# Performance work log

Hardware: AMD Instinct MI355X
Metric: run time of the kernel (lower is better)

## Reference

```python
import jax, jax.numpy as jnp
import numpy as np

TEMPERATURE = 0.5


def setup_inputs() -> dict:
    key = jax.random.key(0)
    k1, k2 = jax.random.split(key)
    emb_i = jax.random.normal(k1, (4096, 512), dtype=jnp.float32)
    emb_j = jax.random.normal(k2, (4096, 512), dtype=jnp.float32)
    return {"emb_i": emb_i, "emb_j": emb_j}


def reference(emb_i, emb_j):
    # NT-Xent (SimCLR) loss, vectorized over the original per-sample python loop.
    N = emb_i.shape[0]
    z_i = emb_i / jnp.linalg.norm(emb_i, axis=1, keepdims=True)
    z_j = emb_j / jnp.linalg.norm(emb_j, axis=1, keepdims=True)
    z = jnp.concatenate([z_i, z_j], axis=0)  # [2N, d]
    # cosine similarity of unit vectors == dot product
    sim = z @ z.T                             # [2N, 2N]
    exp_sim = jnp.exp(sim / TEMPERATURE)
    # denominator excludes self-similarity (the scatter-zero in the original)
    denom = exp_sim.sum(axis=1) - jnp.diagonal(exp_sim)
    idx = jnp.arange(2 * N)
    pos_idx = jnp.concatenate([jnp.arange(N) + N, jnp.arange(N)])
    num = exp_sim[idx, pos_idx]               # positive-pair similarities
    loss = -jnp.log(num / denom)
    return loss.mean()
```

## Files before the change

### kernel.cpp

```cpp
#include <hip/hip_runtime.h>
#include <hip/hip_bf16.h>

typedef __attribute__((ext_vector_type(4))) int i32x4;

#define AS1 __attribute__((address_space(1)))
#define AS3 __attribute__((address_space(3)))

#define DDIM 512
#define BK 64

__global__ __launch_bounds__(256) void norm_pd_kernel(
    const float* __restrict__ ei, const float* __restrict__ ej,
    unsigned char* __restrict__ zq, float* __restrict__ pd,
    float* __restrict__ rowsum, float* __restrict__ out, int N) {
  const int k = blockIdx.x * 4 + (threadIdx.x >> 6);
  const int l = threadIdx.x & 63;

  const float4 a0 = *reinterpret_cast<const float4*>(ei + (size_t)k * DDIM + l * 8);
  const float4 a1 = *reinterpret_cast<const float4*>(ei + (size_t)k * DDIM + l * 8 + 4);
  const float4 b0 = *reinterpret_cast<const float4*>(ej + (size_t)k * DDIM + l * 8);
  const float4 b1 = *reinterpret_cast<const float4*>(ej + (size_t)k * DDIM + l * 8 + 4);

  float sii = a0.x*a0.x + a0.y*a0.y + a0.z*a0.z + a0.w*a0.w
            + a1.x*a1.x + a1.y*a1.y + a1.z*a1.z + a1.w*a1.w;
  float sjj = b0.x*b0.x + b0.y*b0.y + b0.z*b0.z + b0.w*b0.w
            + b1.x*b1.x + b1.y*b1.y + b1.z*b1.z + b1.w*b1.w;
  float sij = a0.x*b0.x + a0.y*b0.y + a0.z*b0.z + a0.w*b0.w
            + a1.x*b1.x + a1.y*b1.y + a1.z*b1.z + a1.w*b1.w;
#pragma unroll
  for (int off = 32; off; off >>= 1) {
    sii += __shfl_xor(sii, off);
    sjj += __shfl_xor(sjj, off);
    sij += __shfl_xor(sij, off);
  }
  const float rsi = rsqrtf(sii), rsj = rsqrtf(sjj);

  unsigned char qa[8], qb[8];
  const float av[8] = {a0.x, a0.y, a0.z, a0.w, a1.x, a1.y, a1.z, a1.w};
  const float bv[8] = {b0.x, b0.y, b0.z, b0.w, b1.x, b1.y, b1.z, b1.w};
#pragma unroll
  for (int i = 0; i < 8; ++i) {
    qa[i] = (unsigned char)((int)rintf(127.0f * av[i] * rsi) & 0xff);
    qb[i] = (unsigned char)((int)rintf(127.0f * bv[i] * rsj) & 0xff);
  }
  *reinterpret_cast<uint2*>(zq + (size_t)k * DDIM + l * 8) =
      *reinterpret_cast<const uint2*>(qa);
  *reinterpret_cast<uint2*>(zq + (size_t)(N + k) * DDIM + l * 8) =
      *reinterpret_cast<const uint2*>(qb);
  if (l == 0) {
    pd[k] = sij * rsi * rsj;
    rowsum[k] = 0.0f;
    rowsum[N + k] = 0.0f;
    if (k == 0) out[0] = 0.0f;
  }
}


#define MFMAI8(A, B, C) __builtin_amdgcn_mfma_i32_16x16x64_i8((A), (B), (C), 0, 0, 0)

__global__ __launch_bounds__(256, 4) void simloss_main(
    const unsigned char* __restrict__ zq, float* __restrict__ rowsum, int nwg) {
  const int orig = blockIdx.x;
  const int q = nwg >> 3, r8 = nwg & 7;
  const int xcd = orig & 7, pos0 = orig >> 3;
  const int t0 = (xcd < r8 ? xcd * (q + 1) : r8 * (q + 1) + (xcd - r8) * q) + pos0;

  const float ff = sqrtf(8.0f * (float)t0 + 1.0f);
  int by = (int)((ff - 1.0f) * 0.5f);
  while ((by + 1) * (by + 2) / 2 <= t0) ++by;
  while (by * (by + 1) / 2 > t0) --by;
  const int bx = t0 - by * (by + 1) / 2;

  const int row0 = bx * 128;
  const int col0 = by * 128;

  __shared__ unsigned char lds[2][2][8192];

  const int tid = threadIdx.x;
  const int w = tid >> 6;
  const int l = tid & 63;
  const int wr = (w >> 1) * 64;
  const int wc = (w & 1) * 64;
  const int lrow = l & 15;
  const int g = l >> 4;

  i32x4 acc[4][4] = {};

  auto stage = [&](int buf, int k0) {
#pragma unroll
    for (int half = 0; half < 2; ++half) {
      const int baserow = half ? col0 : row0;
#pragma unroll
      for (int it = 0; it < 2; ++it) {
        const int pp = it * 256 + tid;
        const int row = pp >> 2;
        const int s = pp & 3;
        const int gs = (s - (row >> 1)) & 3;
        const unsigned char* src = zq + (size_t)(baserow + row) * DDIM + k0 + gs * 16;
        char* dst = (char*)&lds[buf][half][0] + (unsigned)((it * 256 + w * 64) * 16);
        __builtin_amdgcn_global_load_lds((const AS1 void*)src, (AS3 void*)dst, 16, 0, 0);
      }
    }
  };

  auto compute = [&](int buf) {
    const unsigned char* ab = &lds[buf][0][0];
    const unsigned char* bb = &lds[buf][1][0];
    i32x4 Af[4], Bf[4];
#pragma unroll
    for (int mf = 0; mf < 4; ++mf) {
      const int rr = wr + mf * 16 + lrow;
      Af[mf] = *reinterpret_cast<const i32x4*>(ab + rr * 64 + (((g + (rr >> 1)) & 3) << 4));
    }
#pragma unroll
    for (int nf = 0; nf < 4; ++nf) {
      const int cc = wc + nf * 16 + lrow;
      Bf[nf] = *reinterpret_cast<const i32x4*>(bb + cc * 64 + (((g + (cc >> 1)) & 3) << 4));
    }
#pragma unroll
    for (int mf = 0; mf < 4; ++mf)
#pragma unroll
      for (int nf = 0; nf < 4; ++nf)
        acc[mf][nf] = MFMAI8(Af[mf], Bf[nf], acc[mf][nf]);
  };

  stage(0, 0);

#pragma unroll
  for (int t = 0; t < 7; ++t) {
    const int buf = t & 1;
    stage(buf ^ 1, (t + 1) * BK);
    asm volatile("s_waitcnt vmcnt(4)" ::: "memory");
    __builtin_amdgcn_s_barrier();
    compute(buf);
    __builtin_amdgcn_s_barrier();
  }
  asm volatile("s_waitcnt vmcnt(0)" ::: "memory");
  __builtin_amdgcn_s_barrier();
  compute(1);

  const float SC = 2.0f * 1.44269504088896340736f / 16129.0f;
  const int lgrp = l >> 4;
  const int lcol = l & 15;

  float e[4][4][4];
#pragma unroll
  for (int mf = 0; mf < 4; ++mf)
#pragma unroll
    for (int nf = 0; nf < 4; ++nf)
#pragma unroll
      for (int rg = 0; rg < 4; ++rg)
        e[mf][nf][rg] = exp2f((float)acc[mf][nf][rg] * SC);

#pragma unroll
  for (int mf = 0; mf < 4; ++mf) {
    float rs[4];
#pragma unroll
    for (int rg = 0; rg < 4; ++rg) {
      float s = 0.0f;
#pragma unroll
      for (int nf = 0; nf < 4; ++nf) s += e[mf][nf][rg];
      rs[rg] = s;
    }
#pragma unroll
    for (int off = 1; off < 16; off <<= 1) {
#pragma unroll
      for (int rg = 0; rg < 4; ++rg) rs[rg] += __shfl_xor(rs[rg], off);
    }
    if (lcol == 0) {
      const int rowb = row0 + wr + mf * 16 + lgrp * 4;
#pragma unroll
      for (int rg = 0; rg < 4; ++rg) atomicAdd(&rowsum[rowb + rg], rs[rg]);
    }
  }

  if (bx != by) {
#pragma unroll
    for (int nf = 0; nf < 4; ++nf) {
      float cs = 0.0f;
#pragma unroll
      for (int mf = 0; mf < 4; ++mf)
#pragma unroll
        for (int rg = 0; rg < 4; ++rg) cs += e[mf][nf][rg];
      cs += __shfl_xor(cs, 16);
      cs += __shfl_xor(cs, 32);
      if (lgrp == 0) atomicAdd(&rowsum[col0 + wc + nf * 16 + lcol], cs);
    }
  }
}

__global__ __launch_bounds__(1024) void finalize_kernel(
    const float* __restrict__ rowsum, const float* __restrict__ pd,
    float* __restrict__ out, int M, int N) {
  const int i = blockIdx.x * 1024 + threadIdx.x;
  const float E2 = 7.38905609893065f;
  float acc = 0.0f;
  if (i < M) {
    const float denom = rowsum[i] - E2;
    const int kk = (i < N) ? i : (i - N);
    acc = logf(denom) - 2.0f * pd[kk];
  }
#pragma unroll
  for (int off = 32; off; off >>= 1) acc += __shfl_down(acc, off);
  __shared__ float red[16];
  const int t = threadIdx.x;
  if ((t & 63) == 0) red[t >> 6] = acc;
  __syncthreads();
  if (t < 64) {
    float s = (t < 16) ? red[t] : 0.0f;
#pragma unroll
    for (int off = 8; off; off >>= 1) s += __shfl_down(s, off);
    if (t == 0) atomicAdd(out, s / (float)M);
  }
}

extern "C" void kernel_launch(void* const* d_in, const int* in_sizes, int n_in,
                              void* d_out, int out_size, void* d_ws, size_t ws_size,
                              hipStream_t stream) {
  const float* ei = (const float*)d_in[0];
  const float* ej = (const float*)d_in[1];
  float* out = (float*)d_out;

  const int N = in_sizes[0] / DDIM;
  const int M = 2 * N;
  const int NT = M / 128;
  const int NTRI = NT * (NT + 1) / 2;

  char* ws = (char*)d_ws;
  unsigned char* zq = (unsigned char*)ws;
  float* pd = (float*)(ws + (size_t)M * DDIM);
  float* rowsum = (float*)(ws + (size_t)M * DDIM + (size_t)N * 4);

  norm_pd_kernel<<<N / 4, 256, 0, stream>>>(ei, ej, zq, pd, rowsum, out, N);
  simloss_main<<<NTRI, 256, 0, stream>>>(zq, rowsum, NTRI);
  finalize_kernel<<<(M + 1023) / 1024, 1024, 0, stream>>>(rowsum, pd, out, M, N);
}
```

Measured before the change: 44.43 us.

## Split 128x128 tile across 8 waves and fuse exp into row/column sums

Doubles the workgroup to 512 threads (8 waves in a 2x4 grid), so each wave computes a 64x32 sub-tile with half the accumulators. Each thread now issues one async global-to-LDS load per half-tile, and the wait count drops to match. The exponentials are computed inline into the row and column partial sums instead of being held in a 64-float array. This lowers register pressure and raises wave-level parallelism. In exchange, each wave does more LDS A-fragment loads relative to its MFMA work, and barriers must synchronise more waves.

Result: slower. 57.78 us (+30.1%).

```diff
diff --git a/kernel.cpp b/kernel.cpp
--- a/kernel.cpp
+++ b/kernel.cpp
@@ -58,7 +58,7 @@
 
 #define MFMAI8(A, B, C) __builtin_amdgcn_mfma_i32_16x16x64_i8((A), (B), (C), 0, 0, 0)
 
-__global__ __launch_bounds__(256, 4) void simloss_main(
+__global__ __launch_bounds__(512, 8) void simloss_main(
     const unsigned char* __restrict__ zq, float* __restrict__ rowsum, int nwg) {
   const int orig = blockIdx.x;
   const int q = nwg >> 3, r8 = nwg & 7;
@@ -79,48 +79,45 @@
   const int tid = threadIdx.x;
   const int w = tid >> 6;
   const int l = tid & 63;
-  const int wr = (w >> 1) * 64;
-  const int wc = (w & 1) * 64;
+  const int wr = (w >> 2) * 64;
+  const int wc = (w & 3) * 32;
   const int lrow = l & 15;
   const int g = l >> 4;
 
-  i32x4 acc[4][4] = {};
+  i32x4 acc[4][2] = {};
 
   auto stage = [&](int buf, int k0) {
 #pragma unroll
     for (int half = 0; half < 2; ++half) {
       const int baserow = half ? col0 : row0;
-#pragma unroll
-      for (int it = 0; it < 2; ++it) {
-        const int pp = it * 256 + tid;
-        const int row = pp >> 2;
-        const int s = pp & 3;
-        const int gs = (s - (row >> 1)) & 3;
-        const unsigned char* src = zq + (size_t)(baserow + row) * DDIM + k0 + gs * 16;
-        char* dst = (char*)&lds[buf][half][0] + (unsigned)((it * 256 + w * 64) * 16);
-        __builtin_amdgcn_global_load_lds((const AS1 void*)src, (AS3 void*)dst, 16, 0, 0);
-      }
+      const int c = w * 64 + l;
+      const int row = c >> 2;
+      const int s = c & 3;
+      const int gs = (s - (row >> 1)) & 3;
+      const unsigned char* src = zq + (size_t)(baserow + row) * DDIM + k0 + gs * 16;
+      char* dst = (char*)&lds[buf][half][0] + (unsigned)(w * 1024);
+      __builtin_amdgcn_global_load_lds((const AS1 void*)src, (AS3 void*)dst, 16, 0, 0);
     }
   };
 
   auto compute = [&](int buf) {
     const unsigned char* ab = &lds[buf][0][0];
     const unsigned char* bb = &lds[buf][1][0];
-    i32x4 Af[4], Bf[4];
+    i32x4 Af[4], Bf[2];
 #pragma unroll
     for (int mf = 0; mf < 4; ++mf) {
       const int rr = wr + mf * 16 + lrow;
       Af[mf] = *reinterpret_cast<const i32x4*>(ab + rr * 64 + (((g + (rr >> 1)) & 3) << 4));
     }
 #pragma unroll
-    for (int nf = 0; nf < 4; ++nf) {
+    for (int nf = 0; nf < 2; ++nf) {
       const int cc = wc + nf * 16 + lrow;
       Bf[nf] = *reinterpret_cast<const i32x4*>(bb + cc * 64 + (((g + (cc >> 1)) & 3) << 4));
     }
 #pragma unroll
     for (int mf = 0; mf < 4; ++mf)
 #pragma unroll
-      for (int nf = 0; nf < 4; ++nf)
+      for (int nf = 0; nf < 2; ++nf)
         acc[mf][nf] = MFMAI8(Af[mf], Bf[nf], acc[mf][nf]);
   };
 
@@ -130,7 +127,7 @@
   for (int t = 0; t < 7; ++t) {
     const int buf = t & 1;
     stage(buf ^ 1, (t + 1) * BK);
-    asm volatile("s_waitcnt vmcnt(4)" ::: "memory");
+    asm volatile("s_waitcnt vmcnt(2)" ::: "memory");
     __builtin_amdgcn_s_barrier();
     compute(buf);
     __builtin_amdgcn_s_barrier();
@@ -143,24 +140,17 @@
   const int lgrp = l >> 4;
   const int lcol = l & 15;
 
-  float e[4][4][4];
-#pragma unroll
-  for (int mf = 0; mf < 4; ++mf)
-#pragma unroll
-    for (int nf = 0; nf < 4; ++nf)
-#pragma unroll
-      for (int rg = 0; rg < 4; ++rg)
-        e[mf][nf][rg] = exp2f((float)acc[mf][nf][rg] * SC);
-
+  float cs0 = 0.0f, cs1 = 0.0f;
 #pragma unroll
   for (int mf = 0; mf < 4; ++mf) {
     float rs[4];
 #pragma unroll
     for (int rg = 0; rg < 4; ++rg) {
-      float s = 0.0f;
-#pragma unroll
-      for (int nf = 0; nf < 4; ++nf) s += e[mf][nf][rg];
-      rs[rg] = s;
+      const float e0 = exp2f((float)acc[mf][0][rg] * SC);
+      const float e1 = exp2f((float)acc[mf][1][rg] * SC);
+      rs[rg] = e0 + e1;
+      cs0 += e0;
+      cs1 += e1;
     }
 #pragma unroll
     for (int off = 1; off < 16; off <<= 1) {
@@ -175,16 +165,11 @@
   }
 
   if (bx != by) {
-#pragma unroll
-    for (int nf = 0; nf < 4; ++nf) {
-      float cs = 0.0f;
-#pragma unroll
-      for (int mf = 0; mf < 4; ++mf)
-#pragma unroll
-        for (int rg = 0; rg < 4; ++rg) cs += e[mf][nf][rg];
-      cs += __shfl_xor(cs, 16);
-      cs += __shfl_xor(cs, 32);
-      if (lgrp == 0) atomicAdd(&rowsum[col0 + wc + nf * 16 + lcol], cs);
+    cs0 += __shfl_xor(cs0, 16); cs0 += __shfl_xor(cs0, 32);
+    cs1 += __shfl_xor(cs1, 16); cs1 += __shfl_xor(cs1, 32);
+    if (lgrp == 0) {
+      atomicAdd(&rowsum[col0 + wc + lcol], cs0);
+      atomicAdd(&rowsum[col0 + wc + 16 + lcol], cs1);
     }
   }
 }
@@ -232,6 +217,6 @@
   float* rowsum = (float*)(ws + (size_t)M * DDIM + (size_t)N * 4);
 
   norm_pd_kernel<<<N / 4, 256, 0, stream>>>(ei, ej, zq, pd, rowsum, out, N);
-  simloss_main<<<NTRI, 256, 0, stream>>>(zq, rowsum, NTRI);
+  simloss_main<<<NTRI, 512, 0, stream>>>(zq, rowsum, NTRI);
   finalize_kernel<<<(M + 1023) / 1024, 1024, 0, stream>>>(rowsum, pd, out, M, N);
 }
```

## Enlarge similarity tiles to 256x256 with 512-thread blocks and fused epilogue

Applied to the files above, without the earlier changes.

Doubles the output tile of the triangular int8 similarity GEMM from 128x128 to 256x256, using 8 waves of 128x64 subtiles per block, and doubles the LDS staging buffers. Each wave's accumulator grows to 8x4 MFMA tiles. The epilogue now computes exp2 inline and accumulates row and column sums in one pass, dropping the full exp array to save registers. Bigger tiles cut global and LDS reload traffic and per-tile atomics, but give far fewer blocks (528 vs 2080) and lower occupancy, which risks leaving CUs underused.

New measurement: 59.11 us. 33.1% more time.

```diff
diff --git a/kernel.cpp b/kernel.cpp
--- a/kernel.cpp
+++ b/kernel.cpp
@@ -58,7 +58,7 @@
 
 #define MFMAI8(A, B, C) __builtin_amdgcn_mfma_i32_16x16x64_i8((A), (B), (C), 0, 0, 0)
 
-__global__ __launch_bounds__(256, 4) void simloss_main(
+__global__ __launch_bounds__(512, 2) void simloss_main(
     const unsigned char* __restrict__ zq, float* __restrict__ rowsum, int nwg) {
   const int orig = blockIdx.x;
   const int q = nwg >> 3, r8 = nwg & 7;
@@ -71,20 +71,20 @@
   while (by * (by + 1) / 2 > t0) --by;
   const int bx = t0 - by * (by + 1) / 2;
 
-  const int row0 = bx * 128;
-  const int col0 = by * 128;
-
-  __shared__ unsigned char lds[2][2][8192];
+  const int row0 = bx * 256;
+  const int col0 = by * 256;
+
+  __shared__ unsigned char lds[2][2][16384];
 
   const int tid = threadIdx.x;
   const int w = tid >> 6;
   const int l = tid & 63;
-  const int wr = (w >> 1) * 64;
-  const int wc = (w & 1) * 64;
+  const int wm = w >> 2;
+  const int wn = w & 3;
   const int lrow = l & 15;
   const int g = l >> 4;
 
-  i32x4 acc[4][4] = {};
+  i32x4 acc[8][4] = {};
 
   auto stage = [&](int buf, int k0) {
 #pragma unroll
@@ -92,12 +92,12 @@
       const int baserow = half ? col0 : row0;
 #pragma unroll
       for (int it = 0; it < 2; ++it) {
-        const int pp = it * 256 + tid;
+        const int pp = it * 512 + tid;
         const int row = pp >> 2;
         const int s = pp & 3;
         const int gs = (s - (row >> 1)) & 3;
         const unsigned char* src = zq + (size_t)(baserow + row) * DDIM + k0 + gs * 16;
-        char* dst = (char*)&lds[buf][half][0] + (unsigned)((it * 256 + w * 64) * 16);
+        char* dst = (char*)&lds[buf][half][0] + (unsigned)((it * 512 + w * 64) * 16);
         __builtin_amdgcn_global_load_lds((const AS1 void*)src, (AS3 void*)dst, 16, 0, 0);
       }
     }
@@ -106,19 +106,19 @@
   auto compute = [&](int buf) {
     const unsigned char* ab = &lds[buf][0][0];
     const unsigned char* bb = &lds[buf][1][0];
-    i32x4 Af[4], Bf[4];
-#pragma unroll
-    for (int mf = 0; mf < 4; ++mf) {
-      const int rr = wr + mf * 16 + lrow;
+    i32x4 Af[8], Bf[4];
+#pragma unroll
+    for (int mf = 0; mf < 8; ++mf) {
+      const int rr = wm * 128 + mf * 16 + lrow;
       Af[mf] = *reinterpret_cast<const i32x4*>(ab + rr * 64 + (((g + (rr >> 1)) & 3) << 4));
     }
 #pragma unroll
     for (int nf = 0; nf < 4; ++nf) {
-      const int cc = wc + nf * 16 + lrow;
+      const int cc = wn * 64 + nf * 16 + lrow;
       Bf[nf] = *reinterpret_cast<const i32x4*>(bb + cc * 64 + (((g + (cc >> 1)) & 3) << 4));
     }
 #pragma unroll
-    for (int mf = 0; mf < 4; ++mf)
+    for (int mf = 0; mf < 8; ++mf)
 #pragma unroll
       for (int nf = 0; nf < 4; ++nf)
         acc[mf][nf] = MFMAI8(Af[mf], Bf[nf], acc[mf][nf]);
@@ -143,24 +143,20 @@
   const int lgrp = l >> 4;
   const int lcol = l & 15;
 
-  float e[4][4][4];
-#pragma unroll
-  for (int mf = 0; mf < 4; ++mf)
-#pragma unroll
-    for (int nf = 0; nf < 4; ++nf)
-#pragma unroll
-      for (int rg = 0; rg < 4; ++rg)
-        e[mf][nf][rg] = exp2f((float)acc[mf][nf][rg] * SC);
-
-#pragma unroll
-  for (int mf = 0; mf < 4; ++mf) {
+  float cs[4] = {0.0f, 0.0f, 0.0f, 0.0f};
+#pragma unroll
+  for (int mf = 0; mf < 8; ++mf) {
     float rs[4];
 #pragma unroll
-    for (int rg = 0; rg < 4; ++rg) {
-      float s = 0.0f;
-#pragma unroll
-      for (int nf = 0; nf < 4; ++nf) s += e[mf][nf][rg];
-      rs[rg] = s;
+    for (int rg = 0; rg < 4; ++rg) rs[rg] = 0.0f;
+#pragma unroll
+    for (int nf = 0; nf < 4; ++nf) {
+#pragma unroll
+      for (int rg = 0; rg < 4; ++rg) {
+        const float e = exp2f((float)acc[mf][nf][rg] * SC);
+        rs[rg] += e;
+        cs[nf] += e;
+      }
     }
 #pragma unroll
     for (int off = 1; off < 16; off <<= 1) {
@@ -168,7 +164,7 @@
       for (int rg = 0; rg < 4; ++rg) rs[rg] += __shfl_xor(rs[rg], off);
     }
     if (lcol == 0) {
-      const int rowb = row0 + wr + mf * 16 + lgrp * 4;
+      const int rowb = row0 + wm * 128 + mf * 16 + lgrp * 4;
 #pragma unroll
       for (int rg = 0; rg < 4; ++rg) atomicAdd(&rowsum[rowb + rg], rs[rg]);
     }
@@ -177,14 +173,10 @@
   if (bx != by) {
 #pragma unroll
     for (int nf = 0; nf < 4; ++nf) {
-      float cs = 0.0f;
-#pragma unroll
-      for (int mf = 0; mf < 4; ++mf)
-#pragma unroll
-        for (int rg = 0; rg < 4; ++rg) cs += e[mf][nf][rg];
-      cs += __shfl_xor(cs, 16);
-      cs += __shfl_xor(cs, 32);
-      if (lgrp == 0) atomicAdd(&rowsum[col0 + wc + nf * 16 + lcol], cs);
+      float c = cs[nf];
+      c += __shfl_xor(c, 16);
+      c += __shfl_xor(c, 32);
+      if (lgrp == 0) atomicAdd(&rowsum[col0 + wn * 64 + nf * 16 + lcol], c);
     }
   }
 }
@@ -223,7 +215,7 @@
 
   const int N = in_sizes[0] / DDIM;
   const int M = 2 * N;
-  const int NT = M / 128;
+  const int NT = M / 256;
   const int NTRI = NT * (NT + 1) / 2;
 
   char* ws = (char*)d_ws;
@@ -232,6 +224,6 @@
   float* rowsum = (float*)(ws + (size_t)M * DDIM + (size_t)N * 4);
 
   norm_pd_kernel<<<N / 4, 256, 0, stream>>>(ei, ej, zq, pd, rowsum, out, N);
-  simloss_main<<<NTRI, 256, 0, stream>>>(zq, rowsum, NTRI);
+  simloss_main<<<NTRI, 512, 0, stream>>>(zq, rowsum, NTRI);
   finalize_kernel<<<(M + 1023) / 1024, 1024, 0, stream>>>(rowsum, pd, out, M, N);
 }
```
